# Kernel tuning notes

Hardware: AMD Instinct MI355X
Metric: run time of the kernel (lower is better)

The kernel has to match this reference:

```python
import jax, jax.numpy as jnp
import numpy as np

V = 50000
K = 24
NB = 10
P = (K - 1) * 9  # 207 pose-blend coefficients
# canonical SMPL kinematic tree (parent[0] is unused / root)
SMPL_PARENT = np.array([0, 0, 0, 0, 1, 2, 3, 4, 5, 6, 7, 8, 9, 9, 9, 12, 13, 14, 16, 17, 18, 19, 20, 21], dtype=np.int64)


def setup_inputs() -> dict:
    key = jax.random.key(0)
    ks = jax.random.split(key, 8)
    betas = jax.random.normal(ks[0], (NB,), dtype=jnp.float32)
    pose = jax.random.normal(ks[1], (K, 3), dtype=jnp.float32) * 0.3
    trans = jax.random.normal(ks[2], (3,), dtype=jnp.float32)
    shapedirs = jax.random.normal(ks[3], (V, 3, NB), dtype=jnp.float32) * 0.01
    v_template = jax.random.normal(ks[4], (V, 3), dtype=jnp.float32)
    J_regressor = jax.random.uniform(ks[5], (K, V), dtype=jnp.float32)
    J_regressor = J_regressor / jnp.sum(J_regressor, axis=1, keepdims=True)
    weights = jax.random.uniform(ks[6], (V, K), dtype=jnp.float32)
    weights = weights / jnp.sum(weights, axis=1, keepdims=True)
    posedirs = jax.random.normal(ks[7], (V, 3, P), dtype=jnp.float32) * 0.01
    return {"betas": betas, "pose": pose, "trans": trans, "shapedirs": shapedirs,
            "v_template": v_template, "J_regressor": J_regressor, "weights": weights,
            "posedirs": posedirs, "parent": SMPL_PARENT}


def rodrigues(r):
    """Axis-angle [K,3] -> rotation matrices [K,3,3]."""
    theta = jnp.linalg.norm(r + 1e-8, axis=-1, keepdims=True)  # [K,1]
    r_hat = r / theta
    x, y, z = r_hat[:, 0], r_hat[:, 1], r_hat[:, 2]
    zero = jnp.zeros_like(x)
    m = jnp.stack([zero, -z, y, z, zero, -x, -y, x, zero], axis=1).reshape(-1, 3, 3)
    cos = jnp.cos(theta)[:, :, None]
    sin = jnp.sin(theta)[:, :, None]
    eye = jnp.eye(3, dtype=r.dtype)[None]
    outer = r_hat[:, :, None] * r_hat[:, None, :]
    return cos * eye + (1.0 - cos) * outer + sin * m


def smpl_forward(betas, pose, trans, shapedirs, v_template, J_regressor, weights, posedirs, parent):
    parent = np.asarray(parent)
    nJ = parent.shape[0]
    v_shaped = jnp.einsum('vki,i->vk', shapedirs, betas) + v_template  # [V,3]
    J = J_regressor @ v_shaped                                          # [K,3]
    R = rodrigues(pose.reshape(-1, 3))                                  # [K,3,3]
    lrotmin = (R[1:] - jnp.eye(3, dtype=R.dtype)[None]).reshape(-1)     # [207]
    v_posed = v_shaped + jnp.einsum('vkp,p->vk', posedirs, lrotmin)

    bottom = jnp.array([[0.0, 0.0, 0.0, 1.0]], dtype=R.dtype)
    def make_A(Ri, t):  # [3,3],[3] -> [4,4]
        return jnp.concatenate([jnp.concatenate([Ri, t[:, None]], axis=1), bottom], axis=0)

    G = [make_A(R[0], J[0])]
    for i in range(1, nJ):  # fixed 24-joint tree, small static loop
        p = int(parent[i])
        G.append(G[p] @ make_A(R[i], J[i] - J[p]))
    stacked = jnp.stack(G, axis=0)                                      # [K,4,4]

    Jh = jnp.concatenate([J, jnp.zeros((nJ, 1), dtype=J.dtype)], axis=1)[:, :, None]  # [K,4,1]
    corr = stacked @ Jh                                                 # [K,4,1]
    pack = jnp.concatenate([jnp.zeros((nJ, 4, 3), dtype=J.dtype), corr], axis=2)
    results = stacked - pack                                            # [K,4,4]

    T = jnp.einsum('vj,jab->vab', weights, results)                     # [V,4,4]
    rest = jnp.concatenate([v_posed, jnp.ones((v_posed.shape[0], 1), dtype=v_posed.dtype)], axis=1)
    v = jnp.einsum('vab,vb->va', T, rest)[:, :3]
    return v + trans[None, :]


def reference(betas, pose, trans, shapedirs, v_template, J_regressor, weights, posedirs, parent):
    return smpl_forward(betas, pose, trans, shapedirs, v_template, J_regressor, weights, posedirs, parent)
```

## Files before the change

kernel.cpp:

```cpp
#include <hip/hip_runtime.h>

#define NV 50000
#define NJ 24
#define NBETA 10
#define NP 207
#define NROWS 150000
#define ROWGROUPS 37500

#define K1_BLOCKS 196

#define VPB 32
#define RPB 96
#define GPB 24
#define K3_BLOCKS 1563

#define PARTIAL_OFF 0
#define LROT_OFF    14336
#define M_OFF       14592

__device__ const int d_par[NJ] = {0,0,0,0,1,2,3,4,5,6,7,8,9,9,9,12,13,14,16,17,18,19,20,21};
__device__ const int d_lvl[NJ] = {0,1,1,1,2,2,2,3,3,3,4,4,4,4,4,5,5,5,6,6,7,7,8,8};

__global__ __launch_bounds__(256) void k1_partialJ(
    const float* __restrict__ betas, const float* __restrict__ shapedirs,
    const float* __restrict__ v_template, const float* __restrict__ Jreg,
    float* __restrict__ ws)
{
    __shared__ float sd[256 * 30];
    __shared__ float vt[256 * 3];
    __shared__ float bet[NBETA];
    __shared__ float red[4 * 72];

    const int t = threadIdx.x;
    const int blk = blockIdx.x;
    if (t < NBETA) bet[t] = betas[t];

    const int vbase = blk * 256;
    const int nv    = min(256, NV - vbase);
    {
        const int nf4 = (nv * 30) >> 2;
        const float4* sdg = (const float4*)(shapedirs + (size_t)vbase * 30);
        for (int i = t; i < nf4; i += 256) ((float4*)sd)[i] = sdg[i];
        const float* vtg = v_template + (size_t)vbase * 3;
        const int nf3 = nv * 3;
        for (int i = t; i < nf3; i += 256) vt[i] = vtg[i];
    }
    __syncthreads();

    float accJ[72];
#pragma unroll
    for (int q = 0; q < 72; q++) accJ[q] = 0.f;

    const int v = vbase + t;
    if (v < NV) {
        float vs0 = vt[t * 3 + 0], vs1 = vt[t * 3 + 1], vs2 = vt[t * 3 + 2];
#pragma unroll
        for (int i = 0; i < NBETA; i++) {
            const float b = bet[i];
            vs0 += sd[t * 30 + 0 * 10 + i] * b;
            vs1 += sd[t * 30 + 1 * 10 + i] * b;
            vs2 += sd[t * 30 + 2 * 10 + i] * b;
        }
#pragma unroll
        for (int j = 0; j < NJ; j++) {
            const float w = Jreg[(size_t)j * NV + v];
            accJ[j * 3 + 0] += w * vs0;
            accJ[j * 3 + 1] += w * vs1;
            accJ[j * 3 + 2] += w * vs2;
        }
    }

    const int lane = t & 63, wv = t >> 6;
#pragma unroll
    for (int q = 0; q < 72; q++) {
        float x = accJ[q];
#pragma unroll
        for (int m = 1; m < 64; m <<= 1) x += __shfl_xor(x, m);
        if (lane == 0) red[wv * 72 + q] = x;
    }
    __syncthreads();
    if (t < 72)
        ws[PARTIAL_OFF + blk * 72 + t] = red[t] + red[72 + t] + red[144 + t] + red[216 + t];
}

__global__ __launch_bounds__(256) void k2_small(
    const float* __restrict__ pose, float* __restrict__ ws)
{
    __shared__ float Jl[NJ * 3];
    __shared__ float Rl[NJ * 9];
    __shared__ float Gl[NJ * 12];
    const int t = threadIdx.x;

    if (t < 72) {
        float s0 = 0.f, s1 = 0.f;
        for (int b = 0; b < K1_BLOCKS; b += 2) {
            s0 += ws[PARTIAL_OFF + b * 72 + t];
            s1 += ws[PARTIAL_OFF + (b + 1) * 72 + t];
        }
        Jl[t] = s0 + s1;
    }
    __syncthreads();

    if (t < NJ) {
        const float x = pose[t * 3 + 0], y = pose[t * 3 + 1], z = pose[t * 3 + 2];
        const float ex = x + 1e-8f, ey = y + 1e-8f, ez = z + 1e-8f;
        const float theta = sqrtf(ex * ex + ey * ey + ez * ez);
        const float inv = 1.f / theta;
        const float rx = x * inv, ry = y * inv, rz = z * inv;
        const float c = cosf(theta), s = sinf(theta), omc = 1.f - c;
        float R[9];
        R[0] = c + omc * rx * rx;      R[1] = omc * rx * ry - s * rz; R[2] = omc * rx * rz + s * ry;
        R[3] = omc * ry * rx + s * rz; R[4] = c + omc * ry * ry;      R[5] = omc * ry * rz - s * rx;
        R[6] = omc * rz * rx - s * ry; R[7] = omc * rz * ry + s * rx; R[8] = c + omc * rz * rz;
#pragma unroll
        for (int q = 0; q < 9; q++) Rl[t * 9 + q] = R[q];
        if (t >= 1) {
#pragma unroll
            for (int q = 0; q < 9; q++)
                ws[LROT_OFF + (t - 1) * 9 + q] = R[q] - ((q == 0 || q == 4 || q == 8) ? 1.f : 0.f);
        }
    }
    __syncthreads();

    for (int L = 0; L < 9; L++) {
        if (t < NJ && d_lvl[t] == L) {
            if (t == 0) {
#pragma unroll
                for (int r = 0; r < 3; r++) {
                    Gl[r * 4 + 0] = Rl[r * 3 + 0];
                    Gl[r * 4 + 1] = Rl[r * 3 + 1];
                    Gl[r * 4 + 2] = Rl[r * 3 + 2];
                    Gl[r * 4 + 3] = Jl[r];
                }
            } else {
                const int p = d_par[t];
                const float tx = Jl[t * 3 + 0] - Jl[p * 3 + 0];
                const float ty = Jl[t * 3 + 1] - Jl[p * 3 + 1];
                const float tz = Jl[t * 3 + 2] - Jl[p * 3 + 2];
#pragma unroll
                for (int r = 0; r < 3; r++) {
                    const float g0 = Gl[p * 12 + r * 4 + 0];
                    const float g1 = Gl[p * 12 + r * 4 + 1];
                    const float g2 = Gl[p * 12 + r * 4 + 2];
                    const float g3 = Gl[p * 12 + r * 4 + 3];
                    Gl[t * 12 + r * 4 + 0] = g0 * Rl[t * 9 + 0] + g1 * Rl[t * 9 + 3] + g2 * Rl[t * 9 + 6];
                    Gl[t * 12 + r * 4 + 1] = g0 * Rl[t * 9 + 1] + g1 * Rl[t * 9 + 4] + g2 * Rl[t * 9 + 7];
                    Gl[t * 12 + r * 4 + 2] = g0 * Rl[t * 9 + 2] + g1 * Rl[t * 9 + 5] + g2 * Rl[t * 9 + 8];
                    Gl[t * 12 + r * 4 + 3] = g0 * tx + g1 * ty + g2 * tz + g3;
                }
            }
        }
        __syncthreads();
    }

    if (t < NJ) {
        const float jx = Jl[t * 3 + 0], jy = Jl[t * 3 + 1], jz = Jl[t * 3 + 2];
#pragma unroll
        for (int r = 0; r < 3; r++) {
            const float g0 = Gl[t * 12 + r * 4 + 0];
            const float g1 = Gl[t * 12 + r * 4 + 1];
            const float g2 = Gl[t * 12 + r * 4 + 2];
            const float g3 = Gl[t * 12 + r * 4 + 3];
            ws[M_OFF + t * 12 + r * 4 + 0] = g0;
            ws[M_OFF + t * 12 + r * 4 + 1] = g1;
            ws[M_OFF + t * 12 + r * 4 + 2] = g2;
            ws[M_OFF + t * 12 + r * 4 + 3] = g3 - (g0 * jx + g1 * jy + g2 * jz);
        }
    }
}

__global__ __launch_bounds__(256) void k3_fused(
    const float* __restrict__ betas, const float* __restrict__ trans,
    const float* __restrict__ shapedirs, const float* __restrict__ v_template,
    const float* __restrict__ weights, const float* __restrict__ posedirs,
    const float* __restrict__ ws, float* __restrict__ out)
{
    __shared__ float vposed[RPB];
    __shared__ float Ml[288];

    const int t = threadIdx.x;
    const int lane = t & 63, wv = t >> 6;
    const int l16 = lane & 15, g = lane >> 4;
    const int blk = blockIdx.x;

    Ml[t] = ws[M_OFF + t];
    if (t < 32) Ml[256 + t] = ws[M_OFF + 256 + t];

    float lrk[12];
#pragma unroll
    for (int k = 0; k < 12; k++) lrk[k] = ws[LROT_OFF + k * 16 + l16];
    const float lr12 = (l16 < 15) ? ws[LROT_OFF + 192 + l16] : 0.f;
    const float bet  = (l16 < NBETA) ? betas[l16] : 0.f;

    const int gbase = blk * GPB + wv * 6;
    float pv[6][12];
    float tv[6], sv[6];

    if (gbase + 5 < ROWGROUPS) {
#pragma unroll
        for (int i = 0; i < 6; i++) {
            const int row = (gbase + i) * 4 + g;
            const float* pd = posedirs + (size_t)row * NP;
#pragma unroll
            for (int k = 0; k < 12; k++) pv[i][k] = pd[k * 16 + l16];
            tv[i] = (l16 < 15) ? pd[192 + l16] : 0.f;
            sv[i] = (l16 < NBETA) ? shapedirs[(size_t)row * NBETA + l16] : 0.f;
        }
    } else {
#pragma unroll
        for (int i = 0; i < 6; i++) {
            const bool ok = (gbase + i) < ROWGROUPS;
            const int row = ok ? ((gbase + i) * 4 + g) : 0;
            const float* pd = posedirs + (size_t)row * NP;
#pragma unroll
            for (int k = 0; k < 12; k++) pv[i][k] = ok ? pd[k * 16 + l16] : 0.f;
            tv[i] = (ok && l16 < 15) ? pd[192 + l16] : 0.f;
            sv[i] = (ok && l16 < NBETA) ? shapedirs[(size_t)row * NBETA + l16] : 0.f;
        }
    }

    float acc[6];
#pragma unroll
    for (int i = 0; i < 6; i++) {
        float a = tv[i] * lr12 + sv[i] * bet;
#pragma unroll
        for (int k = 0; k < 12; k++) a += pv[i][k] * lrk[k];
        acc[i] = a;
    }
#pragma unroll
    for (int m = 1; m < 16; m <<= 1) {
#pragma unroll
        for (int i = 0; i < 6; i++) acc[i] += __shfl_xor(acc[i], m);
    }
    if (l16 == 0) {
#pragma unroll
        for (int i = 0; i < 6; i++) {
            if (gbase + i < ROWGROUPS)
                vposed[(wv * 6 + i) * 4 + g] = acc[i];
        }
    }
    __syncthreads();

    if (t < VPB) {
        const int v = blk * VPB + t;
        if (v < NV) {
            const float4* w4 = (const float4*)(weights + (size_t)v * 24);
            float wj[24];
#pragma unroll
            for (int q = 0; q < 6; q++) {
                const float4 w = w4[q];
                wj[q * 4 + 0] = w.x; wj[q * 4 + 1] = w.y;
                wj[q * 4 + 2] = w.z; wj[q * 4 + 3] = w.w;
            }
            float T[12];
#pragma unroll
            for (int q = 0; q < 12; q++) T[q] = 0.f;
#pragma unroll
            for (int j = 0; j < NJ; j++) {
                const float w = wj[j];
#pragma unroll
                for (int q = 0; q < 12; q++) T[q] += w * Ml[j * 12 + q];
            }
            const float p0 = vposed[t * 3 + 0] + v_template[(size_t)v * 3 + 0];
            const float p1 = vposed[t * 3 + 1] + v_template[(size_t)v * 3 + 1];
            const float p2 = vposed[t * 3 + 2] + v_template[(size_t)v * 3 + 2];
            out[(size_t)v * 3 + 0] = T[0] * p0 + T[1] * p1 + T[2]  * p2 + T[3]  + trans[0];
            out[(size_t)v * 3 + 1] = T[4] * p0 + T[5] * p1 + T[6]  * p2 + T[7]  + trans[1];
            out[(size_t)v * 3 + 2] = T[8] * p0 + T[9] * p1 + T[10] * p2 + T[11] + trans[2];
        }
    }
}

extern "C" void kernel_launch(void* const* d_in, const int* in_sizes, int n_in,
                              void* d_out, int out_size, void* d_ws, size_t ws_size,
                              hipStream_t stream) {
    const float* betas      = (const float*)d_in[0];
    const float* pose       = (const float*)d_in[1];
    const float* trans      = (const float*)d_in[2];
    const float* shapedirs  = (const float*)d_in[3];
    const float* v_template = (const float*)d_in[4];
    const float* Jreg       = (const float*)d_in[5];
    const float* weights    = (const float*)d_in[6];
    const float* posedirs   = (const float*)d_in[7];
    float* ws  = (float*)d_ws;
    float* out = (float*)d_out;

    k1_partialJ<<<dim3(K1_BLOCKS), dim3(256), 0, stream>>>(betas, shapedirs, v_template, Jreg, ws);
    k2_small<<<dim3(1), dim3(256), 0, stream>>>(pose, ws);
    k3_fused<<<dim3(K3_BLOCKS), dim3(256), 0, stream>>>(
        betas, trans, shapedirs, v_template, weights, posedirs, ws, out);
}
```

Before: 54.89 us.

## Fuse joint regression, kinematic chain and pose blend into one kernel with atomic counter

Merges the joint-regression, joint-transform and pose-blend stages into a single kernel. The first 196 blocks compute partial joint sums and signal completion through an atomic counter, and block 0 spin-waits on it to build the joint transforms. Rodrigues rotations are now recomputed per block in shared memory. Posed vertices go to the output buffer and are skinned in place by a separate kernel. This removes a launch and the serialized single-block stage, but adds a spin-wait that relies on the earlier blocks being scheduled, a memset, and an extra round trip of the output through global memory.

After: 84.45 us. 53.8% more time.

```diff
diff --git a/kernel.cpp b/kernel.cpp
--- a/kernel.cpp
+++ b/kernel.cpp
@@ -8,98 +8,32 @@
 #define ROWGROUPS 37500
 
 #define K1_BLOCKS 196
-
 #define VPB 32
-#define RPB 96
 #define GPB 24
 #define K3_BLOCKS 1563
 
 #define PARTIAL_OFF 0
-#define LROT_OFF    14336
-#define M_OFF       14592
+#define M_OFF       14336
+#define CTR_OFF     14656
 
 __device__ const int d_par[NJ] = {0,0,0,0,1,2,3,4,5,6,7,8,9,9,9,12,13,14,16,17,18,19,20,21};
 __device__ const int d_lvl[NJ] = {0,1,1,1,2,2,2,3,3,3,4,4,4,4,4,5,5,5,6,6,7,7,8,8};
 
-__global__ __launch_bounds__(256) void k1_partialJ(
-    const float* __restrict__ betas, const float* __restrict__ shapedirs,
-    const float* __restrict__ v_template, const float* __restrict__ Jreg,
-    float* __restrict__ ws)
+__global__ __launch_bounds__(256, 4) void k_mega(
+    const float* __restrict__ betas, const float* __restrict__ pose,
+    const float* __restrict__ shapedirs, const float* __restrict__ v_template,
+    const float* __restrict__ Jreg, const float* __restrict__ posedirs,
+    float* __restrict__ ws, float* __restrict__ out)
 {
-    __shared__ float sd[256 * 30];
-    __shared__ float vt[256 * 3];
-    __shared__ float bet[NBETA];
-    __shared__ float red[4 * 72];
+    __shared__ float smem[8448];
+    __shared__ float lrotl[NP];
+    __shared__ float Rl[216];
+    __shared__ float red[288];
 
     const int t = threadIdx.x;
     const int blk = blockIdx.x;
-    if (t < NBETA) bet[t] = betas[t];
-
-    const int vbase = blk * 256;
-    const int nv    = min(256, NV - vbase);
-    {
-        const int nf4 = (nv * 30) >> 2;
-        const float4* sdg = (const float4*)(shapedirs + (size_t)vbase * 30);
-        for (int i = t; i < nf4; i += 256) ((float4*)sd)[i] = sdg[i];
-        const float* vtg = v_template + (size_t)vbase * 3;
-        const int nf3 = nv * 3;
-        for (int i = t; i < nf3; i += 256) vt[i] = vtg[i];
-    }
-    __syncthreads();
-
-    float accJ[72];
-#pragma unroll
-    for (int q = 0; q < 72; q++) accJ[q] = 0.f;
-
-    const int v = vbase + t;
-    if (v < NV) {
-        float vs0 = vt[t * 3 + 0], vs1 = vt[t * 3 + 1], vs2 = vt[t * 3 + 2];
-#pragma unroll
-        for (int i = 0; i < NBETA; i++) {
-            const float b = bet[i];
-            vs0 += sd[t * 30 + 0 * 10 + i] * b;
-            vs1 += sd[t * 30 + 1 * 10 + i] * b;
-            vs2 += sd[t * 30 + 2 * 10 + i] * b;
-        }
-#pragma unroll
-        for (int j = 0; j < NJ; j++) {
-            const float w = Jreg[(size_t)j * NV + v];
-            accJ[j * 3 + 0] += w * vs0;
-            accJ[j * 3 + 1] += w * vs1;
-            accJ[j * 3 + 2] += w * vs2;
-        }
-    }
-
     const int lane = t & 63, wv = t >> 6;
-#pragma unroll
-    for (int q = 0; q < 72; q++) {
-        float x = accJ[q];
-#pragma unroll
-        for (int m = 1; m < 64; m <<= 1) x += __shfl_xor(x, m);
-        if (lane == 0) red[wv * 72 + q] = x;
-    }
-    __syncthreads();
-    if (t < 72)
-        ws[PARTIAL_OFF + blk * 72 + t] = red[t] + red[72 + t] + red[144 + t] + red[216 + t];
-}
-
-__global__ __launch_bounds__(256) void k2_small(
-    const float* __restrict__ pose, float* __restrict__ ws)
-{
-    __shared__ float Jl[NJ * 3];
-    __shared__ float Rl[NJ * 9];
-    __shared__ float Gl[NJ * 12];
-    const int t = threadIdx.x;
-
-    if (t < 72) {
-        float s0 = 0.f, s1 = 0.f;
-        for (int b = 0; b < K1_BLOCKS; b += 2) {
-            s0 += ws[PARTIAL_OFF + b * 72 + t];
-            s1 += ws[PARTIAL_OFF + (b + 1) * 72 + t];
-        }
-        Jl[t] = s0 + s1;
-    }
-    __syncthreads();
+    const int l16 = lane & 15, g = lane >> 4;
 
     if (t < NJ) {
         const float x = pose[t * 3 + 0], y = pose[t * 3 + 1], z = pose[t * 3 + 2];
@@ -108,88 +42,154 @@
         const float inv = 1.f / theta;
         const float rx = x * inv, ry = y * inv, rz = z * inv;
         const float c = cosf(theta), s = sinf(theta), omc = 1.f - c;
-        float R[9];
-        R[0] = c + omc * rx * rx;      R[1] = omc * rx * ry - s * rz; R[2] = omc * rx * rz + s * ry;
-        R[3] = omc * ry * rx + s * rz; R[4] = c + omc * ry * ry;      R[5] = omc * ry * rz - s * rx;
-        R[6] = omc * rz * rx - s * ry; R[7] = omc * rz * ry + s * rx; R[8] = c + omc * rz * rz;
-#pragma unroll
-        for (int q = 0; q < 9; q++) Rl[t * 9 + q] = R[q];
-        if (t >= 1) {
-#pragma unroll
-            for (int q = 0; q < 9; q++)
-                ws[LROT_OFF + (t - 1) * 9 + q] = R[q] - ((q == 0 || q == 4 || q == 8) ? 1.f : 0.f);
-        }
+        Rl[t * 9 + 0] = c + omc * rx * rx;      Rl[t * 9 + 1] = omc * rx * ry - s * rz;
+        Rl[t * 9 + 2] = omc * rx * rz + s * ry; Rl[t * 9 + 3] = omc * ry * rx + s * rz;
+        Rl[t * 9 + 4] = c + omc * ry * ry;      Rl[t * 9 + 5] = omc * ry * rz - s * rx;
+        Rl[t * 9 + 6] = omc * rz * rx - s * ry; Rl[t * 9 + 7] = omc * rz * ry + s * rx;
+        Rl[t * 9 + 8] = c + omc * rz * rz;
     }
     __syncthreads();
-
-    for (int L = 0; L < 9; L++) {
-        if (t < NJ && d_lvl[t] == L) {
-            if (t == 0) {
-#pragma unroll
-                for (int r = 0; r < 3; r++) {
-                    Gl[r * 4 + 0] = Rl[r * 3 + 0];
-                    Gl[r * 4 + 1] = Rl[r * 3 + 1];
-                    Gl[r * 4 + 2] = Rl[r * 3 + 2];
-                    Gl[r * 4 + 3] = Jl[r];
+    if (t >= 9 && t < 216) {
+        const int q = t % 9;
+        lrotl[t - 9] = Rl[t] - ((q == 0 || q == 4 || q == 8) ? 1.f : 0.f);
+    }
+
+    if (blk < K1_BLOCKS) {
+        float* sd = smem;
+        float* vt = smem + 7680;
+        const int vbase = blk * 256;
+        const int nv    = min(256, NV - vbase);
+        {
+            const int nf4 = (nv * 30) >> 2;
+            const float4* sdg = (const float4*)(shapedirs + (size_t)vbase * 30);
+            for (int i = t; i < nf4; i += 256) ((float4*)sd)[i] = sdg[i];
+            const float* vtg = v_template + (size_t)vbase * 3;
+            const int nf3 = nv * 3;
+            for (int i = t; i < nf3; i += 256) vt[i] = vtg[i];
+        }
+        __syncthreads();
+
+        float accJ[72];
+#pragma unroll
+        for (int q = 0; q < 72; q++) accJ[q] = 0.f;
+
+        const int v = vbase + t;
+        if (v < NV) {
+            float vs0 = vt[t * 3 + 0], vs1 = vt[t * 3 + 1], vs2 = vt[t * 3 + 2];
+#pragma unroll
+            for (int i = 0; i < NBETA; i++) {
+                const float b = betas[i];
+                vs0 += sd[t * 30 + 0 * 10 + i] * b;
+                vs1 += sd[t * 30 + 1 * 10 + i] * b;
+                vs2 += sd[t * 30 + 2 * 10 + i] * b;
+            }
+#pragma unroll
+            for (int j = 0; j < NJ; j++) {
+                const float w = Jreg[(size_t)j * NV + v];
+                accJ[j * 3 + 0] += w * vs0;
+                accJ[j * 3 + 1] += w * vs1;
+                accJ[j * 3 + 2] += w * vs2;
+            }
+        }
+
+#pragma unroll
+        for (int q = 0; q < 72; q++) {
+            float x = accJ[q];
+#pragma unroll
+            for (int m = 1; m < 64; m <<= 1) x += __shfl_xor(x, m);
+            if (lane == 0) red[wv * 72 + q] = x;
+        }
+        __syncthreads();
+        if (t < 72)
+            ws[PARTIAL_OFF + blk * 72 + t] = red[t] + red[72 + t] + red[144 + t] + red[216 + t];
+        __threadfence();
+        __syncthreads();
+        if (t == 0)
+            __hip_atomic_fetch_add((unsigned int*)(ws + CTR_OFF), 1u,
+                                   __ATOMIC_RELEASE, __HIP_MEMORY_SCOPE_AGENT);
+    }
+
+    if (blk == 0) {
+        if (t == 0) {
+            while (__hip_atomic_load((const unsigned int*)(ws + CTR_OFF),
+                                     __ATOMIC_ACQUIRE, __HIP_MEMORY_SCOPE_AGENT)
+                   < (unsigned int)K1_BLOCKS) {
+                __builtin_amdgcn_s_sleep(8);
+            }
+        }
+        __syncthreads();
+        __threadfence();
+
+        float* Jl = smem;
+        float* cs = smem + 128;
+        float* Gl = smem + 512;
+
+        if (t < 216) {
+            const int q = t % 72, chunk = t / 72;
+            const int b0 = chunk * 66;
+            const int b1 = min(K1_BLOCKS, b0 + 66);
+            float s = 0.f;
+            volatile const float* vp = ws + PARTIAL_OFF;
+            for (int b = b0; b < b1; b++) s += vp[b * 72 + q];
+            cs[chunk * 72 + q] = s;
+        }
+        __syncthreads();
+        if (t < 72) Jl[t] = cs[t] + cs[72 + t] + cs[144 + t];
+        __syncthreads();
+
+        for (int L = 0; L < 9; L++) {
+            if (t < NJ && d_lvl[t] == L) {
+                if (t == 0) {
+#pragma unroll
+                    for (int r = 0; r < 3; r++) {
+                        Gl[r * 4 + 0] = Rl[r * 3 + 0];
+                        Gl[r * 4 + 1] = Rl[r * 3 + 1];
+                        Gl[r * 4 + 2] = Rl[r * 3 + 2];
+                        Gl[r * 4 + 3] = Jl[r];
+                    }
+                } else {
+                    const int p = d_par[t];
+                    const float tx = Jl[t * 3 + 0] - Jl[p * 3 + 0];
+                    const float ty = Jl[t * 3 + 1] - Jl[p * 3 + 1];
+                    const float tz = Jl[t * 3 + 2] - Jl[p * 3 + 2];
+#pragma unroll
+                    for (int r = 0; r < 3; r++) {
+                        const float g0 = Gl[p * 12 + r * 4 + 0];
+                        const float g1 = Gl[p * 12 + r * 4 + 1];
+                        const float g2 = Gl[p * 12 + r * 4 + 2];
+                        const float g3 = Gl[p * 12 + r * 4 + 3];
+                        Gl[t * 12 + r * 4 + 0] = g0 * Rl[t * 9 + 0] + g1 * Rl[t * 9 + 3] + g2 * Rl[t * 9 + 6];
+                        Gl[t * 12 + r * 4 + 1] = g0 * Rl[t * 9 + 1] + g1 * Rl[t * 9 + 4] + g2 * Rl[t * 9 + 7];
+                        Gl[t * 12 + r * 4 + 2] = g0 * Rl[t * 9 + 2] + g1 * Rl[t * 9 + 5] + g2 * Rl[t * 9 + 8];
+                        Gl[t * 12 + r * 4 + 3] = g0 * tx + g1 * ty + g2 * tz + g3;
+                    }
                 }
-            } else {
-                const int p = d_par[t];
-                const float tx = Jl[t * 3 + 0] - Jl[p * 3 + 0];
-                const float ty = Jl[t * 3 + 1] - Jl[p * 3 + 1];
-                const float tz = Jl[t * 3 + 2] - Jl[p * 3 + 2];
-#pragma unroll
-                for (int r = 0; r < 3; r++) {
-                    const float g0 = Gl[p * 12 + r * 4 + 0];
-                    const float g1 = Gl[p * 12 + r * 4 + 1];
-                    const float g2 = Gl[p * 12 + r * 4 + 2];
-                    const float g3 = Gl[p * 12 + r * 4 + 3];
-                    Gl[t * 12 + r * 4 + 0] = g0 * Rl[t * 9 + 0] + g1 * Rl[t * 9 + 3] + g2 * Rl[t * 9 + 6];
-                    Gl[t * 12 + r * 4 + 1] = g0 * Rl[t * 9 + 1] + g1 * Rl[t * 9 + 4] + g2 * Rl[t * 9 + 7];
-                    Gl[t * 12 + r * 4 + 2] = g0 * Rl[t * 9 + 2] + g1 * Rl[t * 9 + 5] + g2 * Rl[t * 9 + 8];
-                    Gl[t * 12 + r * 4 + 3] = g0 * tx + g1 * ty + g2 * tz + g3;
-                }
-            }
-        }
-        __syncthreads();
-    }
-
-    if (t < NJ) {
-        const float jx = Jl[t * 3 + 0], jy = Jl[t * 3 + 1], jz = Jl[t * 3 + 2];
-#pragma unroll
-        for (int r = 0; r < 3; r++) {
-            const float g0 = Gl[t * 12 + r * 4 + 0];
-            const float g1 = Gl[t * 12 + r * 4 + 1];
-            const float g2 = Gl[t * 12 + r * 4 + 2];
-            const float g3 = Gl[t * 12 + r * 4 + 3];
-            ws[M_OFF + t * 12 + r * 4 + 0] = g0;
-            ws[M_OFF + t * 12 + r * 4 + 1] = g1;
-            ws[M_OFF + t * 12 + r * 4 + 2] = g2;
-            ws[M_OFF + t * 12 + r * 4 + 3] = g3 - (g0 * jx + g1 * jy + g2 * jz);
-        }
-    }
-}
-
-__global__ __launch_bounds__(256) void k3_fused(
-    const float* __restrict__ betas, const float* __restrict__ trans,
-    const float* __restrict__ shapedirs, const float* __restrict__ v_template,
-    const float* __restrict__ weights, const float* __restrict__ posedirs,
-    const float* __restrict__ ws, float* __restrict__ out)
-{
-    __shared__ float vposed[RPB];
-    __shared__ float Ml[288];
-
-    const int t = threadIdx.x;
-    const int lane = t & 63, wv = t >> 6;
-    const int l16 = lane & 15, g = lane >> 4;
-    const int blk = blockIdx.x;
-
-    Ml[t] = ws[M_OFF + t];
-    if (t < 32) Ml[256 + t] = ws[M_OFF + 256 + t];
+            }
+            __syncthreads();
+        }
+
+        if (t < NJ) {
+            const float jx = Jl[t * 3 + 0], jy = Jl[t * 3 + 1], jz = Jl[t * 3 + 2];
+#pragma unroll
+            for (int r = 0; r < 3; r++) {
+                const float g0 = Gl[t * 12 + r * 4 + 0];
+                const float g1 = Gl[t * 12 + r * 4 + 1];
+                const float g2 = Gl[t * 12 + r * 4 + 2];
+                const float g3 = Gl[t * 12 + r * 4 + 3];
+                ws[M_OFF + t * 12 + r * 4 + 0] = g0;
+                ws[M_OFF + t * 12 + r * 4 + 1] = g1;
+                ws[M_OFF + t * 12 + r * 4 + 2] = g2;
+                ws[M_OFF + t * 12 + r * 4 + 3] = g3 - (g0 * jx + g1 * jy + g2 * jz);
+            }
+        }
+    }
+
+    __syncthreads();
 
     float lrk[12];
 #pragma unroll
-    for (int k = 0; k < 12; k++) lrk[k] = ws[LROT_OFF + k * 16 + l16];
-    const float lr12 = (l16 < 15) ? ws[LROT_OFF + 192 + l16] : 0.f;
+    for (int k = 0; k < 12; k++) lrk[k] = lrotl[k * 16 + l16];
+    const float lr12 = (l16 < 15) ? lrotl[192 + l16] : 0.f;
     const float bet  = (l16 < NBETA) ? betas[l16] : 0.f;
 
     const int gbase = blk * GPB + wv * 6;
@@ -235,40 +235,53 @@
     if (l16 == 0) {
 #pragma unroll
         for (int i = 0; i < 6; i++) {
-            if (gbase + i < ROWGROUPS)
-                vposed[(wv * 6 + i) * 4 + g] = acc[i];
-        }
-    }
+            const int grp = gbase + i;
+            if (grp < ROWGROUPS) {
+                const int row = grp * 4 + g;
+                out[row] = acc[i] + v_template[row];
+            }
+        }
+    }
+}
+
+__global__ __launch_bounds__(256) void k_skin(
+    const float* __restrict__ trans, const float* __restrict__ weights,
+    const float* __restrict__ ws, float* __restrict__ out)
+{
+    __shared__ float Ml[288];
+    const int t = threadIdx.x;
+    Ml[t] = ws[M_OFF + t];
+    if (t < 32) Ml[256 + t] = ws[M_OFF + 256 + t];
     __syncthreads();
 
-    if (t < VPB) {
-        const int v = blk * VPB + t;
-        if (v < NV) {
-            const float4* w4 = (const float4*)(weights + (size_t)v * 24);
-            float wj[24];
-#pragma unroll
-            for (int q = 0; q < 6; q++) {
-                const float4 w = w4[q];
-                wj[q * 4 + 0] = w.x; wj[q * 4 + 1] = w.y;
-                wj[q * 4 + 2] = w.z; wj[q * 4 + 3] = w.w;
-            }
-            float T[12];
-#pragma unroll
-            for (int q = 0; q < 12; q++) T[q] = 0.f;
-#pragma unroll
-            for (int j = 0; j < NJ; j++) {
-                const float w = wj[j];
-#pragma unroll
-                for (int q = 0; q < 12; q++) T[q] += w * Ml[j * 12 + q];
-            }
-            const float p0 = vposed[t * 3 + 0] + v_template[(size_t)v * 3 + 0];
-            const float p1 = vposed[t * 3 + 1] + v_template[(size_t)v * 3 + 1];
-            const float p2 = vposed[t * 3 + 2] + v_template[(size_t)v * 3 + 2];
-            out[(size_t)v * 3 + 0] = T[0] * p0 + T[1] * p1 + T[2]  * p2 + T[3]  + trans[0];
-            out[(size_t)v * 3 + 1] = T[4] * p0 + T[5] * p1 + T[6]  * p2 + T[7]  + trans[1];
-            out[(size_t)v * 3 + 2] = T[8] * p0 + T[9] * p1 + T[10] * p2 + T[11] + trans[2];
-        }
-    }
+    const int v = blockIdx.x * 256 + t;
+    if (v >= NV) return;
+
+    const float4* w4 = (const float4*)(weights + (size_t)v * 24);
+    float wj[24];
+#pragma unroll
+    for (int q = 0; q < 6; q++) {
+        const float4 w = w4[q];
+        wj[q * 4 + 0] = w.x; wj[q * 4 + 1] = w.y;
+        wj[q * 4 + 2] = w.z; wj[q * 4 + 3] = w.w;
+    }
+
+    float T[12];
+#pragma unroll
+    for (int q = 0; q < 12; q++) T[q] = 0.f;
+#pragma unroll
+    for (int j = 0; j < NJ; j++) {
+        const float w = wj[j];
+#pragma unroll
+        for (int q = 0; q < 12; q++) T[q] += w * Ml[j * 12 + q];
+    }
+
+    const float p0 = out[(size_t)v * 3 + 0];
+    const float p1 = out[(size_t)v * 3 + 1];
+    const float p2 = out[(size_t)v * 3 + 2];
+    out[(size_t)v * 3 + 0] = T[0] * p0 + T[1] * p1 + T[2]  * p2 + T[3]  + trans[0];
+    out[(size_t)v * 3 + 1] = T[4] * p0 + T[5] * p1 + T[6]  * p2 + T[7]  + trans[1];
+    out[(size_t)v * 3 + 2] = T[8] * p0 + T[9] * p1 + T[10] * p2 + T[11] + trans[2];
 }
 
 extern "C" void kernel_launch(void* const* d_in, const int* in_sizes, int n_in,
@@ -285,8 +298,9 @@
     float* ws  = (float*)d_ws;
     float* out = (float*)d_out;
 
-    k1_partialJ<<<dim3(K1_BLOCKS), dim3(256), 0, stream>>>(betas, shapedirs, v_template, Jreg, ws);
-    k2_small<<<dim3(1), dim3(256), 0, stream>>>(pose, ws);
-    k3_fused<<<dim3(K3_BLOCKS), dim3(256), 0, stream>>>(
-        betas, trans, shapedirs, v_template, weights, posedirs, ws, out);
+    hipMemsetAsync((char*)d_ws + CTR_OFF * sizeof(float), 0, sizeof(unsigned int), stream);
+
+    k_mega<<<dim3(K3_BLOCKS), dim3(256), 0, stream>>>(
+        betas, pose, shapedirs, v_template, Jreg, posedirs, ws, out);
+    k_skin<<<dim3((NV + 255) / 256), dim3(256), 0, stream>>>(trans, weights, ws, out);
 }
```
